# Optimization experiments

Hardware: AMD Instinct MI355X
Metric: run time of the kernel (lower is better)

## Reference

```python
import jax, jax.numpy as jnp
import numpy as np

PATCH, WIN = 3, 7


def _unfold(x, k):
    # torch F.unfold(x, k, padding=k//2), stride 1 -> [b, c, k*k, h, w]
    # channel-major ordering (c slowest, then kernel row, then kernel col)
    pad = k // 2
    b, c, h, w = x.shape
    xp = jnp.pad(x, ((0, 0), (0, 0), (pad, pad), (pad, pad)))
    return jnp.stack([xp[:, :, i:i + h, j:j + w]
                      for i in range(k) for j in range(k)], axis=2)


def _conv3(x, w, b=None):
    y = jax.lax.conv_general_dilated(x, w, (1, 1), [(1, 1), (1, 1)],
                                     dimension_numbers=('NCHW', 'OIHW', 'NCHW'))
    if b is not None:
        y = y + b[None, :, None, None]
    return y


def _head(u_feat, pan_feat, w_phi, w_theta, w_g, p, ws):
    # SelfAttention: windowed/patch neighborhood attention
    b, c, h, w = pan_feat.shape
    phi = jnp.einsum('oi,bihw->bohw', w_phi, pan_feat)
    theta = jnp.einsum('oi,bihw->bohw', w_theta, pan_feat)
    thp = _unfold(theta, p).reshape(b, c * p * p, h, w)        # [b,D,h,w]
    php = _unfold(phi, p).reshape(b, c * p * p, h, w)          # [b,D,h,w]
    phw = _unfold(php, ws)                                     # [b,D,K,h,w], K=ws*ws
    att = jax.nn.softmax(jnp.einsum('bdhw,bdkhw->bhwk', thp, phw), axis=-1)
    g = jnp.einsum('oi,bihw->bohw', w_g, u_feat)
    gw = _unfold(g, ws)                                        # [b,cu,K,h,w]
    return jnp.einsum('bhwk,bckhw->bchw', att, gw)


def _forward(u, pan, w_nlu, w_nlpan, g_phi, g_theta, g_g, s_phi, s_theta, s_g,
             m_phi, m_theta, m_g, mlp_w, mlp_b, w_resu, w_respan,
             rb0_w1, rb0_b1, rb0_w2, rb0_b2, rb1_w1, rb1_b1, rb1_w2, rb1_b2,
             rb2_w1, rb2_b1, rb2_w2, rb2_b2, w_recon):
    uf = _conv3(u, w_nlu)      # [b,5,h,w]
    pf = _conv3(pan, w_nlpan)  # [b,3,h,w]
    h1 = _head(uf, pf, g_phi, g_theta, g_g, PATCH, WIN)
    h2 = _head(uf, uf, s_phi, s_theta, s_g, 1, WIN)
    h3 = _head(uf, jnp.concatenate([uf, pf], axis=1), m_phi, m_theta, m_g, PATCH, WIN)
    # mlp: Linear(3,1) over stacked heads (last dim of size 3)
    att = h1 * mlp_w[0, 0] + h2 * mlp_w[0, 1] + h3 * mlp_w[0, 2] + mlp_b[0]
    ru = _conv3(u, w_resu)
    rp = _conv3(pan, w_respan)
    x = jnp.concatenate([att, ru, rp], axis=1)  # [b, fc+10, h, w]
    rbs = [(rb0_w1, rb0_b1, rb0_w2, rb0_b2),
           (rb1_w1, rb1_b1, rb1_w2, rb1_b2),
           (rb2_w1, rb2_b1, rb2_w2, rb2_b2)]
    for w1, b1, w2, b2 in rbs:
        f = jax.nn.relu(_conv3(x, w1, b1))
        f = _conv3(f, w2, b2)
        x = jax.nn.relu(f + x)
    return _conv3(x, w_recon)


def setup_inputs() -> dict:
    key = jax.random.key(0)
    ks = jax.random.split(key, 32)
    def n(i, shape, s=0.1):
        return jax.random.normal(ks[i], shape, dtype=jnp.float32) * s
    B, H, W = 1, 128, 128
    FC = 32
    C = FC + 10
    inp = {
        'u': jax.random.normal(ks[0], (B, 8, H, W), dtype=jnp.float32),
        'pan': jax.random.normal(ks[1], (B, 1, H, W), dtype=jnp.float32),
        'w_nlu': n(2, (5, 8, 3, 3)),
        'w_nlpan': n(3, (3, 1, 3, 3)),
        'g_phi': n(4, (3, 3)), 'g_theta': n(5, (3, 3)), 'g_g': n(6, (5, 5)),
        's_phi': n(7, (5, 5)), 's_theta': n(8, (5, 5)), 's_g': n(9, (5, 5)),
        'm_phi': n(10, (8, 8)), 'm_theta': n(11, (8, 8)), 'm_g': n(12, (5, 5)),
        'mlp_w': n(13, (1, 3), 0.5), 'mlp_b': n(14, (1,), 0.1),
        'w_resu': n(15, (FC, 8, 3, 3)), 'w_respan': n(16, (5, 1, 3, 3)),
        'w_recon': n(17, (8, C, 3, 3)),
    }
    k = 18
    for i in range(3):
        inp[f'rb{i}_w1'] = n(k, (C, C, 3, 3))
        inp[f'rb{i}_b1'] = n(k + 1, (C,), 0.01)
        inp[f'rb{i}_w2'] = n(k + 2, (C, C, 3, 3))
        inp[f'rb{i}_b2'] = n(k + 3, (C,), 0.01)
        k += 4
    return inp


def reference(u, pan, w_nlu, w_nlpan, g_phi, g_theta, g_g, s_phi, s_theta, s_g,
              m_phi, m_theta, m_g, mlp_w, mlp_b, w_resu, w_respan,
              rb0_w1, rb0_b1, rb0_w2, rb0_b2, rb1_w1, rb1_b1, rb1_w2, rb1_b2,
              rb2_w1, rb2_b1, rb2_w2, rb2_b2, w_recon):
    return _forward(u, pan, w_nlu, w_nlpan, g_phi, g_theta, g_g, s_phi, s_theta,
                    s_g, m_phi, m_theta, m_g, mlp_w, mlp_b, w_resu, w_respan,
                    rb0_w1, rb0_b1, rb0_w2, rb0_b2, rb1_w1, rb1_b1, rb1_w2,
                    rb1_b2, rb2_w1, rb2_b1, rb2_w2, rb2_b2, w_recon)
```

## Files before the change

kernel.cpp:

```cpp
#include <hip/hip_runtime.h>


#define DEV __device__ __forceinline__
typedef float f32x4 __attribute__((ext_vector_type(4)));
typedef __bf16 bf16x8 __attribute__((ext_vector_type(8)));
typedef unsigned short u16;
typedef unsigned int u32;

constexpr int N = 128 * 128;

constexpr int OFF_PHI1 =   0 * N;
constexpr int OFF_TH1  =   3 * N;
constexpr int OFF_PHI2 =   6 * N;
constexpr int OFF_TH2  =  11 * N;
constexpr int OFF_PHI3 =  16 * N;
constexpr int OFF_TH3  =  24 * N;
constexpr int OFF_G1   =  32 * N;
constexpr int OFF_G2   =  37 * N;
constexpr int OFF_G3   =  42 * N;
constexpr int OFF_X    =  47 * N;
constexpr int OFF_OH1  =  89 * N;
constexpr int OFF_OH2  =  94 * N;
constexpr int OFF_OH3  =  99 * N;
constexpr int XPLANE   = 130 * 136;
constexpr int OFF_XPAD = 110 * N;
constexpr int OFF_FPAD = 133 * N;
constexpr int OFF_SLAB = 156 * N;
constexpr int OFF_BTAB = 160 * N;
constexpr int SLAB_RB  = 18432;
constexpr int SLAB_RC  = 110592;
constexpr int SLAB_TOT = 116736;
constexpr int ZPB      = 528;
constexpr int ZTOT     = 2 * 42 * ZPB;
constexpr int WPREP_TOT = 384 + SLAB_TOT + ZTOT;
constexpr int WPREP_BLK = (WPREP_TOT + 255) / 256;

DEV bool inb(int y, int x) { return (unsigned)y < 128u && (unsigned)x < 128u; }
DEV u16 f2bf(float f) {
    unsigned u = __float_as_uint(f);
    return (u16)((u + 0x7fffu + ((u >> 16) & 1u)) >> 16);
}

struct PrepArgs {
    const float* u;    const float* pan;  const float* wnlu; const float* wnlpan;
    const float* gphi; const float* gth;  const float* gg;   const float* sphi;
    const float* sth;  const float* sg;   const float* mphi; const float* mth;
    const float* mg;
    const float* w[7];
};

__global__ __launch_bounds__(256) void prep_k(PrepArgs pa, float* __restrict__ ws,
                                              u16* __restrict__ slab,
                                              u16* __restrict__ btab,
                                              u16* __restrict__ xpad,
                                              u16* __restrict__ fpad) {
    const int bid = blockIdx.x, t = threadIdx.x;
    if (bid < 128) {
        const int p = (bid & 63) * 256 + t;
        const int y = p >> 7, x = p & 127;

        float uv[8][9];
#pragma unroll
        for (int ic = 0; ic < 8; ++ic)
#pragma unroll
            for (int i = 0; i < 3; ++i)
#pragma unroll
                for (int j = 0; j < 3; ++j) {
                    int yy = y + i - 1, xx = x + j - 1;
                    uv[ic][i * 3 + j] =
                        inb(yy, xx) ? pa.u[ic * N + yy * 128 + xx] : 0.f;
                }
        float uf[5] = {0, 0, 0, 0, 0};
#pragma unroll
        for (int ic = 0; ic < 8; ++ic)
#pragma unroll
            for (int k = 0; k < 9; ++k)
#pragma unroll
                for (int o = 0; o < 5; ++o)
                    uf[o] = fmaf(uv[ic][k], pa.wnlu[(o * 8 + ic) * 9 + k], uf[o]);

        if (bid < 64) {
#pragma unroll
            for (int o = 0; o < 5; ++o) {
                float a = 0, b = 0, c1 = 0, c2 = 0, c3 = 0;
#pragma unroll
                for (int i = 0; i < 5; ++i) {
                    a  = fmaf(pa.sphi[o * 5 + i], uf[i], a);
                    b  = fmaf(pa.sth [o * 5 + i], uf[i], b);
                    c1 = fmaf(pa.gg  [o * 5 + i], uf[i], c1);
                    c2 = fmaf(pa.sg  [o * 5 + i], uf[i], c2);
                    c3 = fmaf(pa.mg  [o * 5 + i], uf[i], c3);
                }
                ws[OFF_PHI2 + o * N + p] = a;
                ws[OFF_TH2  + o * N + p] = b;
                ws[OFF_G1   + o * N + p] = c1;
                ws[OFF_G2   + o * N + p] = c2;
                ws[OFF_G3   + o * N + p] = c3;
            }
        } else {
            float pv[9];
#pragma unroll
            for (int i = 0; i < 3; ++i)
#pragma unroll
                for (int j = 0; j < 3; ++j) {
                    int yy = y + i - 1, xx = x + j - 1;
                    pv[i * 3 + j] = inb(yy, xx) ? pa.pan[yy * 128 + xx] : 0.f;
                }
            float pf[3] = {0, 0, 0};
#pragma unroll
            for (int k = 0; k < 9; ++k)
#pragma unroll
                for (int o = 0; o < 3; ++o)
                    pf[o] = fmaf(pv[k], pa.wnlpan[o * 9 + k], pf[o]);
            float cat[8] = {uf[0], uf[1], uf[2], uf[3], uf[4],
                            pf[0], pf[1], pf[2]};
#pragma unroll
            for (int o = 0; o < 3; ++o) {
                float a = 0, b = 0;
#pragma unroll
                for (int i = 0; i < 3; ++i) {
                    a = fmaf(pa.gphi[o * 3 + i], pf[i], a);
                    b = fmaf(pa.gth [o * 3 + i], pf[i], b);
                }
                ws[OFF_PHI1 + o * N + p] = a;
                ws[OFF_TH1  + o * N + p] = b;
            }
#pragma unroll
            for (int o = 0; o < 8; ++o) {
                float a = 0, b = 0;
#pragma unroll
                for (int i = 0; i < 8; ++i) {
                    a = fmaf(pa.mphi[o * 8 + i], cat[i], a);
                    b = fmaf(pa.mth [o * 8 + i], cat[i], b);
                }
                ws[OFF_PHI3 + o * N + p] = a;
                ws[OFF_TH3  + o * N + p] = b;
            }
        }
        return;
    }

    int idx = (bid - 128) * 256 + t;
    if (idx >= WPREP_TOT) return;
    if (idx < 384) {
        u16 v = 0;
        if (idx < 378) {
            int ic = idx / 9, tau = idx - ic * 9;
            v = (u16)(ic * 120 + (tau / 3) * 40 + (tau % 3));
        }
        btab[idx] = v;
        return;
    }
    idx -= 384;
    if (idx < SLAB_TOT) {
        const float* W;
        int mt, ks, lane, j, ocv;
        if (idx < SLAB_RC) {
            int cv = idx / SLAB_RB, r = idx - cv * SLAB_RB;
            mt = r / 6144; r -= mt * 6144;
            ks = r / 512;  r -= ks * 512;
            lane = r / 8;  j = r - lane * 8;
            W = pa.w[cv]; ocv = 42;
        } else {
            int r = idx - SLAB_RC;
            mt = 0;
            ks = r / 512;  r -= ks * 512;
            lane = r / 8;  j = r - lane * 8;
            W = pa.w[6]; ocv = 8;
        }
        int k  = ks * 32 + (lane >> 4) * 8 + j;
        int oc = mt * 16 + (lane & 15);
        u16 v = 0;
        if (k < 378 && oc < ocv) {
            int ic = k / 9, tau = k - ic * 9;
            v = f2bf(W[(oc * 42 + ic) * 9 + tau]);
        }
        slab[idx] = v;
        return;
    }
    idx -= SLAB_TOT;
    u16* buf = (idx < 42 * ZPB) ? xpad : fpad;
    int e = (idx < 42 * ZPB) ? idx : idx - 42 * ZPB;
    int plane = e / ZPB, rem = e - plane * ZPB;
    int row, col;
    if (rem < 136)      { row = 0;             col = rem; }
    else if (rem < 272) { row = 129;           col = rem - 136; }
    else if (rem < 400) { row = 1 + rem - 272; col = 0; }
    else                { row = 1 + rem - 400; col = 129; }
    buf[plane * XPLANE + row * 136 + col] = 0;
}

template <int C, int P>
DEV void head_tile(const float* __restrict__ phi, const float* __restrict__ theta,
                   const float* __restrict__ g, float* __restrict__ oh,
                   float* __restrict__ smem, int ty0, int tx0, int t) {
    constexpr int PR  = P / 2;
    constexpr int H3  = 3 + PR;
    constexpr int W   = 6 + P;
    constexpr int TTH = 8 + 2 * PR, TTW = 8 + 2 * PR;
    constexpr int PTH = 8 + 2 * H3, PTW = 8 + 2 * H3;
    constexpr int GTH = 14, GTW = 14;

    float* sT = smem;
    float* sP = sT + C * TTH * TTW;
    float* sG = sP + C * PTH * PTW;

#pragma unroll
    for (int c = 0; c < C; ++c)
#pragma unroll
        for (int base = 0; base < TTH * TTW; base += 128) {
            int i = base + t;
            if (i < TTH * TTW) {
                int r = i / TTW, cc = i - r * TTW;
                int gy = ty0 - PR + r, gx = tx0 - PR + cc;
                sT[c * TTH * TTW + i] =
                    inb(gy, gx) ? theta[c * N + gy * 128 + gx] : 0.f;
            }
        }
#pragma unroll
    for (int c = 0; c < C; ++c)
#pragma unroll
        for (int base = 0; base < PTH * PTW; base += 128) {
            int i = base + t;
            if (i < PTH * PTW) {
                int r = i / PTW, cc = i - r * PTW;
                int gy = ty0 - H3 + r, gx = tx0 - H3 + cc;
                sP[c * PTH * PTW + i] =
                    inb(gy, gx) ? phi[c * N + gy * 128 + gx] : 0.f;
            }
        }
#pragma unroll
    for (int c = 0; c < 5; ++c)
#pragma unroll
        for (int base = 0; base < GTH * GTW; base += 128) {
            int i = base + t;
            if (i < GTH * GTW) {
                int r = i / GTW, cc = i - r * GTW;
                int gy = ty0 - 3 + r, gx = tx0 - 3 + cc;
                sG[c * GTH * GTW + i] =
                    inb(gy, gx) ? g[c * N + gy * 128 + gx] : 0.f;
            }
        }
    __syncthreads();

    const int wave = t >> 6, lane = t & 63, m = lane >> 5;
    const int pidx = (lane & 31) | (wave << 5);
    const int py = pidx >> 3, px = pidx & 7;
    const int gy = ty0 + py, gx = tx0 + px;
    const int dbase = m * 3;

    float s[28];
#pragma unroll
    for (int k = 0; k < 28; ++k) s[k] = 0.f;

    for (int c = 0; c < C; ++c) {
        const float* tc = sT + c * TTH * TTW;
        const float* pc = sP + c * PTH * PTW;
        float T[P][P];
#pragma unroll
        for (int i = 0; i < P; ++i)
#pragma unroll
            for (int j = 0; j < P; ++j)
                T[i][j] = tc[(py + i) * TTW + px + j];
        float R[P][W];
#pragma unroll
        for (int r = 0; r < P; ++r)
#pragma unroll
            for (int w = 0; w < W; ++w)
                R[r][w] = pc[(py + dbase + r) * PTW + px + w];
#pragma unroll
        for (int dd = 0; dd < 4; ++dd) {
#pragma unroll
            for (int dx = 0; dx < 7; ++dx) {
                float a = 0.f;
#pragma unroll
                for (int i = 0; i < P; ++i)
#pragma unroll
                    for (int j = 0; j < P; ++j)
                        a = fmaf(T[i][j], R[i][dx + j], a);
                s[dd * 7 + dx] += a;
            }
            if (dd < 3) {
#pragma unroll
                for (int r = 0; r < P - 1; ++r)
#pragma unroll
                    for (int w = 0; w < W; ++w) R[r][w] = R[r + 1][w];
                int row = py + dbase + dd + P;
#pragma unroll
                for (int w = 0; w < W; ++w)
                    R[P - 1][w] = pc[row * PTW + px + w];
            }
        }
    }
#pragma unroll
    for (int k = 0; k < 28; ++k) {
        int d = dbase + k / 7, dx = k % 7;
        if (!inb(gy + d - 3, gx + dx - 3)) s[k] = 0.f;
    }
    const bool half0 = (m == 0);
    float mx = -3.0e38f;
#pragma unroll
    for (int k = 0; k < 28; ++k) {
        bool own = half0 || (k >= 7);
        mx = own ? fmaxf(mx, s[k]) : mx;
    }
    mx = fmaxf(mx, __shfl_xor(mx, 32));
    float sum = 0.f;
#pragma unroll
    for (int k = 0; k < 28; ++k) {
        bool own = half0 || (k >= 7);
        float e = own ? __expf(s[k] - mx) : 0.f;
        s[k] = e;
        sum += e;
    }
    sum += __shfl_xor(sum, 32);

    float o[5] = {0, 0, 0, 0, 0};
#pragma unroll
    for (int k = 0; k < 28; ++k) {
        int d = dbase + k / 7, dx = k % 7;
        int gr = (py + d) * GTW + px + dx;
#pragma unroll
        for (int c5 = 0; c5 < 5; ++c5)
            o[c5] = fmaf(s[k], sG[c5 * GTH * GTW + gr], o[c5]);
    }
#pragma unroll
    for (int c5 = 0; c5 < 5; ++c5) o[c5] += __shfl_xor(o[c5], 32);

    if (half0) {
        float inv = 1.f / sum;
        int p = gy * 128 + gx;
#pragma unroll
        for (int c5 = 0; c5 < 5; ++c5) oh[c5 * N + p] = o[c5] * inv;
    }
}

__global__ __launch_bounds__(128) void heads_k(float* __restrict__ ws) {
    __shared__ float smem[3828];
    const int t = threadIdx.x;
    const int ty0 = (blockIdx.x >> 4) * 8, tx0 = (blockIdx.x & 15) * 8;
    if (blockIdx.y == 0)
        head_tile<3, 3>(ws + OFF_PHI1, ws + OFF_TH1, ws + OFF_G1, ws + OFF_OH1,
                        smem, ty0, tx0, t);
    else if (blockIdx.y == 1)
        head_tile<5, 1>(ws + OFF_PHI2, ws + OFF_TH2, ws + OFF_G2, ws + OFF_OH2,
                        smem, ty0, tx0, t);
    else
        head_tile<8, 3>(ws + OFF_PHI3, ws + OFF_TH3, ws + OFF_G3, ws + OFF_OH3,
                        smem, ty0, tx0, t);
}

__global__ __launch_bounds__(256, 2) void assemble_k(
    const float* __restrict__ u, const float* __restrict__ pan,
    const float* __restrict__ wres, const float* __restrict__ wrp,
    const float* __restrict__ mlpw, const float* __restrict__ mlpb,
    float* __restrict__ ws, u16* __restrict__ xpad) {
    const int p = blockIdx.x * 256 + threadIdx.x;
    const int y = p >> 7, x = p & 127;
    const int padp = (y + 1) * 136 + (x + 1);
    float* xb = ws + OFF_X;

    if (blockIdx.y == 0) {
        const float w0 = mlpw[0], w1 = mlpw[1], w2 = mlpw[2];
        const float bb = mlpb[0];
#pragma unroll
        for (int c = 0; c < 5; ++c) {
            float a = ws[OFF_OH1 + c * N + p] * w0 +
                      ws[OFF_OH2 + c * N + p] * w1 +
                      ws[OFF_OH3 + c * N + p] * w2 + bb;
            xb[c * N + p] = a;
            xpad[c * XPLANE + padp] = f2bf(a);
        }
        float pv[9];
#pragma unroll
        for (int i = 0; i < 3; ++i)
#pragma unroll
            for (int j = 0; j < 3; ++j) {
                int yy = y + i - 1, xx = x + j - 1;
                pv[i * 3 + j] = inb(yy, xx) ? pan[yy * 128 + xx] : 0.f;
            }
        float a5[5] = {0, 0, 0, 0, 0};
#pragma unroll
        for (int k = 0; k < 9; ++k)
#pragma unroll
            for (int o = 0; o < 5; ++o)
                a5[o] = fmaf(pv[k], wrp[o * 9 + k], a5[o]);
#pragma unroll
        for (int o = 0; o < 5; ++o) {
            xb[(37 + o) * N + p] = a5[o];
            xpad[(37 + o) * XPLANE + padp] = f2bf(a5[o]);
        }
    } else {
        const int ob = (blockIdx.y - 1) * 8;
        float uv[8][9];
#pragma unroll
        for (int ic = 0; ic < 8; ++ic)
#pragma unroll
            for (int i = 0; i < 3; ++i)
#pragma unroll
                for (int j = 0; j < 3; ++j) {
                    int yy = y + i - 1, xx = x + j - 1;
                    uv[ic][i * 3 + j] =
                        inb(yy, xx) ? u[ic * N + yy * 128 + xx] : 0.f;
                }
        float acc[8] = {0, 0, 0, 0, 0, 0, 0, 0};
#pragma unroll
        for (int ic = 0; ic < 8; ++ic)
#pragma unroll
            for (int k = 0; k < 9; ++k)
#pragma unroll
                for (int o = 0; o < 8; ++o)
                    acc[o] = fmaf(uv[ic][k], wres[((ob + o) * 8 + ic) * 9 + k],
                                  acc[o]);
#pragma unroll
        for (int o = 0; o < 8; ++o) {
            xb[(5 + ob + o) * N + p] = acc[o];
            xpad[(5 + ob + o) * XPLANE + padp] = f2bf(acc[o]);
        }
    }
}

template <int MT, int OCV, bool BIAS, bool RELU, bool SKIP, bool WF32, bool WPAD>
__global__ __launch_bounds__(128, 1) void convm_k(
    const u16* __restrict__ xin, const u16* __restrict__ slab,
    const u16* __restrict__ btab, const float* __restrict__ bs,
    const float* __restrict__ skip, float* __restrict__ of32,
    u16* __restrict__ opad) {
    __shared__ __align__(16) u16 sX[5040];
    __shared__ __align__(16) u16 sBt[384];
    const int t = threadIdx.x;
    const int y = blockIdx.x >> 2, x0 = (blockIdx.x & 3) << 5;

    const u16* srcbase = xin + y * 136 + x0;
#pragma unroll
    for (int it = 0; it < 5; ++it) {
        int c = it * 128 + t;
        if (c < 630) {
            int row = c / 5, slot = c - row * 5;
            int ic = row / 3, r = row - ic * 3;
            uint4 v = *((const uint4*)(srcbase + ic * XPLANE + r * 136) + slot);
            *(uint4*)(sX + row * 40 + slot * 8) = v;
        }
    }
#pragma unroll
    for (int it = 0; it < 3; ++it) sBt[it * 128 + t] = btab[it * 128 + t];
    __syncthreads();

    const int lane = t & 63, wave = t >> 6;
    const int quad = lane >> 4, col = lane & 15;
    const int ncol = wave * 16 + col;

    union AB { uint4 u; bf16x8 b; };
    AB a[MT][12];
#pragma unroll
    for (int mt = 0; mt < MT; ++mt)
#pragma unroll
        for (int ks = 0; ks < 12; ++ks)
            a[mt][ks].u = ((const uint4*)slab)[(mt * 12 + ks) * 64 + lane];

    f32x4 acc[MT];
#pragma unroll
    for (int mt = 0; mt < MT; ++mt) acc[mt] = {0.f, 0.f, 0.f, 0.f};

#pragma unroll
    for (int ks = 0; ks < 12; ++ks) {
        union { uint4 u; u16 s[8]; } off;
        off.u = *(const uint4*)(sBt + ks * 32 + quad * 8);
        union { u16 s[8]; bf16x8 b; } bv;
#pragma unroll
        for (int j = 0; j < 8; ++j) bv.s[j] = sX[off.s[j] + ncol];
#pragma unroll
        for (int mt = 0; mt < MT; ++mt)
            acc[mt] = __builtin_amdgcn_mfma_f32_16x16x32_bf16(
                a[mt][ks].b, bv.b, acc[mt], 0, 0, 0);
    }

    const int xg = x0 + ncol;
    const int px = y * 128 + xg;
    const int padp = (y + 1) * 136 + (xg + 1);
#pragma unroll
    for (int mt = 0; mt < MT; ++mt)
#pragma unroll
        for (int reg = 0; reg < 4; ++reg) {
            int oc = mt * 16 + quad * 4 + reg;
            if (oc < OCV) {
                float v = acc[mt][reg];
                if (BIAS) v += bs[oc];
                if (SKIP) v += skip[oc * N + px];
                if (RELU) v = fmaxf(v, 0.f);
                if (WF32) of32[oc * N + px] = v;
                if (WPAD) opad[oc * XPLANE + padp] = f2bf(v);
            }
        }
}

extern "C" void kernel_launch(void* const* d_in, const int* in_sizes, int n_in,
                              void* d_out, int out_size, void* d_ws, size_t ws_size,
                              hipStream_t stream) {
    (void)in_sizes; (void)n_in; (void)out_size; (void)ws_size;
    float* ws = (float*)d_ws;
    float* out = (float*)d_out;

    PrepArgs pa;
    pa.u      = (const float*)d_in[0];
    pa.pan    = (const float*)d_in[1];
    pa.wnlu   = (const float*)d_in[2];
    pa.wnlpan = (const float*)d_in[3];
    pa.gphi   = (const float*)d_in[4];
    pa.gth    = (const float*)d_in[5];
    pa.gg     = (const float*)d_in[6];
    pa.sphi   = (const float*)d_in[7];
    pa.sth    = (const float*)d_in[8];
    pa.sg     = (const float*)d_in[9];
    pa.mphi   = (const float*)d_in[10];
    pa.mth    = (const float*)d_in[11];
    pa.mg     = (const float*)d_in[12];
    pa.w[0]   = (const float*)d_in[18];
    pa.w[1]   = (const float*)d_in[20];
    pa.w[2]   = (const float*)d_in[22];
    pa.w[3]   = (const float*)d_in[24];
    pa.w[4]   = (const float*)d_in[26];
    pa.w[5]   = (const float*)d_in[28];
    pa.w[6]   = (const float*)d_in[17];

    const float* mlpw = (const float*)d_in[13];
    const float* mlpb = (const float*)d_in[14];
    const float* wres = (const float*)d_in[15];
    const float* wrp  = (const float*)d_in[16];

    u16* xpad = (u16*)(ws + OFF_XPAD);
    u16* fpad = (u16*)(ws + OFF_FPAD);
    u16* slab = (u16*)(ws + OFF_SLAB);
    u16* btab = (u16*)(ws + OFF_BTAB);

    prep_k<<<128 + WPREP_BLK, 256, 0, stream>>>(pa, ws, slab, btab, xpad, fpad);
    heads_k<<<dim3(256, 3), 128, 0, stream>>>(ws);
    assemble_k<<<dim3(64, 5), 256, 0, stream>>>(pa.u, pa.pan, wres, wrp, mlpw,
                                                mlpb, ws, xpad);

    for (int r = 0; r < 3; ++r) {
        const float* b1 = (const float*)d_in[19 + 4 * r];
        const float* b2 = (const float*)d_in[21 + 4 * r];
        convm_k<3, 42, true, true, false, false, true>
            <<<512, 128, 0, stream>>>(xpad, slab + (2 * r) * SLAB_RB, btab, b1,
                                      nullptr, nullptr, fpad);
        convm_k<3, 42, true, true, true, true, true>
            <<<512, 128, 0, stream>>>(fpad, slab + (2 * r + 1) * SLAB_RB, btab,
                                      b2, ws + OFF_X, ws + OFF_X, xpad);
    }
    convm_k<1, 8, false, false, false, true, false>
        <<<512, 128, 0, stream>>>(xpad, slab + SLAB_RC, btab, nullptr, nullptr,
                                  out, nullptr);
}
```

Baseline: 210.9 us.

## Fuse residual-block conv pairs and merge heads with assemble kernel

```diff
diff --git a/kernel.cpp b/kernel.cpp
--- a/kernel.cpp
+++ b/kernel.cpp
@@ -19,20 +19,17 @@
 constexpr int OFF_G2   =  37 * N;
 constexpr int OFF_G3   =  42 * N;
 constexpr int OFF_X    =  47 * N;
-constexpr int OFF_OH1  =  89 * N;
-constexpr int OFF_OH2  =  94 * N;
-constexpr int OFF_OH3  =  99 * N;
-constexpr int XPLANE   = 130 * 136;
-constexpr int OFF_XPAD = 110 * N;
-constexpr int OFF_FPAD = 133 * N;
-constexpr int OFF_SLAB = 156 * N;
-constexpr int OFF_BTAB = 160 * N;
+constexpr int XPLANE   = 132 * 144;
+constexpr int OFF_XPA  = 110 * N;
+constexpr int OFF_XPB  = 135 * N;
+constexpr int OFF_SLAB = 160 * N;
+constexpr int OFF_BTAB = 164 * N;
 constexpr int SLAB_RB  = 18432;
 constexpr int SLAB_RC  = 110592;
 constexpr int SLAB_TOT = 116736;
-constexpr int ZPB      = 528;
+constexpr int ZPB      = 2624;
 constexpr int ZTOT     = 2 * 42 * ZPB;
-constexpr int WPREP_TOT = 384 + SLAB_TOT + ZTOT;
+constexpr int WPREP_TOT = 1152 + SLAB_TOT + ZTOT;
 constexpr int WPREP_BLK = (WPREP_TOT + 255) / 256;
 
 DEV bool inb(int y, int x) { return (unsigned)y < 128u && (unsigned)x < 128u; }
@@ -52,8 +49,8 @@
 __global__ __launch_bounds__(256) void prep_k(PrepArgs pa, float* __restrict__ ws,
                                               u16* __restrict__ slab,
                                               u16* __restrict__ btab,
-                                              u16* __restrict__ xpad,
-                                              u16* __restrict__ fpad) {
+                                              u16* __restrict__ xpa,
+                                              u16* __restrict__ xpb) {
     const int bid = blockIdx.x, t = threadIdx.x;
     if (bid < 128) {
         const int p = (bid & 63) * 256 + t;
@@ -142,16 +139,19 @@
 
     int idx = (bid - 128) * 256 + t;
     if (idx >= WPREP_TOT) return;
-    if (idx < 384) {
+    if (idx < 1152) {
+        int which = idx / 384, k = idx - which * 384;
         u16 v = 0;
-        if (idx < 378) {
-            int ic = idx / 9, tau = idx - ic * 9;
-            v = (u16)(ic * 120 + (tau / 3) * 40 + (tau % 3));
+        if (k < 378) {
+            int ic = k / 9, tau = k - ic * 9, i = tau / 3, j = tau - i * 3;
+            if (which == 0)      v = (u16)(ic * 360 + i * 72 + j);
+            else if (which == 1) v = (u16)(ic * 216 + i * 72 + j);
+            else                 v = (u16)(ic * 120 + i * 40 + j + 1);
         }
         btab[idx] = v;
         return;
     }
-    idx -= 384;
+    idx -= 1152;
     if (idx < SLAB_TOT) {
         const float* W;
         int mt, ks, lane, j, ocv;
@@ -179,21 +179,27 @@
         return;
     }
     idx -= SLAB_TOT;
-    u16* buf = (idx < 42 * ZPB) ? xpad : fpad;
+    u16* buf = (idx < 42 * ZPB) ? xpa : xpb;
     int e = (idx < 42 * ZPB) ? idx : idx - 42 * ZPB;
     int plane = e / ZPB, rem = e - plane * ZPB;
     int row, col;
-    if (rem < 136)      { row = 0;             col = rem; }
-    else if (rem < 272) { row = 129;           col = rem - 136; }
-    else if (rem < 400) { row = 1 + rem - 272; col = 0; }
-    else                { row = 1 + rem - 400; col = 129; }
-    buf[plane * XPLANE + row * 136 + col] = 0;
+    if (rem < 576) {
+        int rr = rem / 144;
+        row = (rr < 2) ? rr : rr + 128;
+        col = rem - rr * 144;
+    } else {
+        int r2 = rem - 576;
+        row = 2 + r2 / 16;
+        int ci = r2 & 15;
+        col = (ci < 2) ? ci : 128 + ci;
+    }
+    buf[plane * XPLANE + row * 144 + col] = 0;
 }
 
 template <int C, int P>
 DEV void head_tile(const float* __restrict__ phi, const float* __restrict__ theta,
-                   const float* __restrict__ g, float* __restrict__ oh,
-                   float* __restrict__ smem, int ty0, int tx0, int t) {
+                   const float* __restrict__ g, float* __restrict__ smem,
+                   int ty0, int tx0, int t, float ohv[5]) {
     constexpr int PR  = P / 2;
     constexpr int H3  = 3 + PR;
     constexpr int W   = 6 + P;
@@ -205,6 +211,7 @@
     float* sP = sT + C * TTH * TTW;
     float* sG = sP + C * PTH * PTW;
 
+    __syncthreads();
 #pragma unroll
     for (int c = 0; c < C; ++c)
 #pragma unroll
@@ -327,56 +334,81 @@
 #pragma unroll
     for (int c5 = 0; c5 < 5; ++c5) o[c5] += __shfl_xor(o[c5], 32);
 
-    if (half0) {
-        float inv = 1.f / sum;
-        int p = gy * 128 + gx;
-#pragma unroll
-        for (int c5 = 0; c5 < 5; ++c5) oh[c5 * N + p] = o[c5] * inv;
-    }
+    float inv = 1.f / sum;
+#pragma unroll
+    for (int c5 = 0; c5 < 5; ++c5) ohv[c5] = o[c5] * inv;
 }
 
-__global__ __launch_bounds__(128) void heads_k(float* __restrict__ ws) {
-    __shared__ float smem[3828];
-    const int t = threadIdx.x;
-    const int ty0 = (blockIdx.x >> 4) * 8, tx0 = (blockIdx.x & 15) * 8;
-    if (blockIdx.y == 0)
-        head_tile<3, 3>(ws + OFF_PHI1, ws + OFF_TH1, ws + OFF_G1, ws + OFF_OH1,
-                        smem, ty0, tx0, t);
-    else if (blockIdx.y == 1)
-        head_tile<5, 1>(ws + OFF_PHI2, ws + OFF_TH2, ws + OFF_G2, ws + OFF_OH2,
-                        smem, ty0, tx0, t);
-    else
-        head_tile<8, 3>(ws + OFF_PHI3, ws + OFF_TH3, ws + OFF_G3, ws + OFF_OH3,
-                        smem, ty0, tx0, t);
-}
-
-__global__ __launch_bounds__(256, 2) void assemble_k(
+__global__ __launch_bounds__(128) void headsasm_k(
     const float* __restrict__ u, const float* __restrict__ pan,
     const float* __restrict__ wres, const float* __restrict__ wrp,
     const float* __restrict__ mlpw, const float* __restrict__ mlpb,
     float* __restrict__ ws, u16* __restrict__ xpad) {
-    const int p = blockIdx.x * 256 + threadIdx.x;
-    const int y = p >> 7, x = p & 127;
-    const int padp = (y + 1) * 136 + (x + 1);
+    __shared__ float smem[3828];
+    const int t = threadIdx.x;
+    const int ty0 = (blockIdx.x >> 4) * 8, tx0 = (blockIdx.x & 15) * 8;
+
+    float h1[5], h2[5], h3[5];
+    head_tile<3, 3>(ws + OFF_PHI1, ws + OFF_TH1, ws + OFF_G1, smem, ty0, tx0,
+                    t, h1);
+    head_tile<5, 1>(ws + OFF_PHI2, ws + OFF_TH2, ws + OFF_G2, smem, ty0, tx0,
+                    t, h2);
+    head_tile<8, 3>(ws + OFF_PHI3, ws + OFF_TH3, ws + OFF_G3, smem, ty0, tx0,
+                    t, h3);
+
+    const int wave = t >> 6, lane = t & 63, m = lane >> 5;
+    const int pidx = (lane & 31) | (wave << 5);
+    const int py = pidx >> 3, px8 = pidx & 7;
+    const int gy = ty0 + py, gx = tx0 + px8;
+    const int p = gy * 128 + gx;
+    const int padp = (gy + 2) * 144 + (gx + 2);
     float* xb = ws + OFF_X;
 
-    if (blockIdx.y == 0) {
+    if (m == 0) {
         const float w0 = mlpw[0], w1 = mlpw[1], w2 = mlpw[2];
         const float bb = mlpb[0];
 #pragma unroll
         for (int c = 0; c < 5; ++c) {
-            float a = ws[OFF_OH1 + c * N + p] * w0 +
-                      ws[OFF_OH2 + c * N + p] * w1 +
-                      ws[OFF_OH3 + c * N + p] * w2 + bb;
+            float a = h1[c] * w0 + h2[c] * w1 + h3[c] * w2 + bb;
             xb[c * N + p] = a;
             xpad[c * XPLANE + padp] = f2bf(a);
         }
+    }
+    float uv[8][9];
+#pragma unroll
+    for (int ic = 0; ic < 8; ++ic)
+#pragma unroll
+        for (int i = 0; i < 3; ++i)
+#pragma unroll
+            for (int j = 0; j < 3; ++j) {
+                int yy = gy + i - 1, xx = gx + j - 1;
+                uv[ic][i * 3 + j] = inb(yy, xx) ? u[ic * N + yy * 128 + xx] : 0.f;
+            }
+    const int ob = m * 16;
+    float acc[16];
+#pragma unroll
+    for (int o = 0; o < 16; ++o) acc[o] = 0.f;
+#pragma unroll
+    for (int ic = 0; ic < 8; ++ic)
+#pragma unroll
+        for (int k = 0; k < 9; ++k)
+#pragma unroll
+            for (int o = 0; o < 16; ++o)
+                acc[o] = fmaf(uv[ic][k], wres[((ob + o) * 8 + ic) * 9 + k],
+                              acc[o]);
+#pragma unroll
+    for (int o = 0; o < 16; ++o) {
+        int ch = 5 + ob + o;
+        xb[ch * N + p] = acc[o];
+        xpad[ch * XPLANE + padp] = f2bf(acc[o]);
+    }
+    if (m == 1) {
         float pv[9];
 #pragma unroll
         for (int i = 0; i < 3; ++i)
 #pragma unroll
             for (int j = 0; j < 3; ++j) {
-                int yy = y + i - 1, xx = x + j - 1;
+                int yy = gy + i - 1, xx = gx + j - 1;
                 pv[i * 3 + j] = inb(yy, xx) ? pan[yy * 128 + xx] : 0.f;
             }
         float a5[5] = {0, 0, 0, 0, 0};
@@ -387,63 +419,152 @@
                 a5[o] = fmaf(pv[k], wrp[o * 9 + k], a5[o]);
 #pragma unroll
         for (int o = 0; o < 5; ++o) {
-            xb[(37 + o) * N + p] = a5[o];
-            xpad[(37 + o) * XPLANE + padp] = f2bf(a5[o]);
-        }
-    } else {
-        const int ob = (blockIdx.y - 1) * 8;
-        float uv[8][9];
-#pragma unroll
-        for (int ic = 0; ic < 8; ++ic)
-#pragma unroll
-            for (int i = 0; i < 3; ++i)
-#pragma unroll
-                for (int j = 0; j < 3; ++j) {
-                    int yy = y + i - 1, xx = x + j - 1;
-                    uv[ic][i * 3 + j] =
-                        inb(yy, xx) ? u[ic * N + yy * 128 + xx] : 0.f;
+            int ch = 37 + o;
+            xb[ch * N + p] = a5[o];
+            xpad[ch * XPLANE + padp] = f2bf(a5[o]);
+        }
+    }
+}
+
+__global__ __launch_bounds__(128, 1) void rbfused_k(
+    const u16* __restrict__ xin, u16* __restrict__ xout,
+    const u16* __restrict__ slab1, const u16* __restrict__ slab2,
+    const u16* __restrict__ btab, const float* __restrict__ b1,
+    const float* __restrict__ b2, float* __restrict__ xskip) {
+    __shared__ __align__(16) u16 xT[15120];
+    __shared__ __align__(16) u16 fT[9072];
+    __shared__ __align__(16) u16 sBtA[384], sBtB[384];
+    __shared__ float sB1[42], sB2[42];
+    const int t = threadIdx.x;
+    const int y = blockIdx.x >> 1, x0 = (blockIdx.x & 1) << 6;
+
+#pragma unroll
+    for (int it = 0; it < 15; ++it) {
+        int c = it * 128 + t;
+        if (c < 1890) {
+            int row = c / 9, slot = c - row * 9;
+            int ic = row / 5, r5 = row - ic * 5;
+            uint4 v = *((const uint4*)(xin + ic * XPLANE + (y + r5) * 144 + x0)
+                        + slot);
+            *(uint4*)(xT + ic * 360 + r5 * 72 + slot * 8) = v;
+        }
+    }
+#pragma unroll
+    for (int it = 0; it < 3; ++it) sBtA[it * 128 + t] = btab[it * 128 + t];
+#pragma unroll
+    for (int it = 0; it < 3; ++it) sBtB[it * 128 + t] = btab[384 + it * 128 + t];
+    if (t < 42) { sB1[t] = b1[t]; sB2[t] = b2[t]; }
+    __syncthreads();
+
+    const int lane = t & 63, wave = t >> 6;
+    const int quad = lane >> 4, col = lane & 15;
+
+    union AB { uint4 u; bf16x8 b; };
+    AB a[3][12];
+#pragma unroll
+    for (int mt = 0; mt < 3; ++mt)
+#pragma unroll
+        for (int ks = 0; ks < 12; ++ks)
+            a[mt][ks].u = ((const uint4*)slab1)[(mt * 12 + ks) * 64 + lane];
+
+    for (int tl = wave; tl < 13; tl += 2) {
+        int n = tl * 16 + col;
+        bool valid = n < 198;
+        int r = n / 66, cc = n - r * 66;
+        int base = valid ? r * 72 + cc : 0;
+        f32x4 acc[3];
+#pragma unroll
+        for (int mt = 0; mt < 3; ++mt) acc[mt] = {0.f, 0.f, 0.f, 0.f};
+#pragma unroll
+        for (int ks = 0; ks < 12; ++ks) {
+            union { uint4 u; u16 s[8]; } off;
+            off.u = *(const uint4*)(sBtA + ks * 32 + quad * 8);
+            union { u16 s[8]; bf16x8 b; } bv;
+#pragma unroll
+            for (int j = 0; j < 8; ++j) bv.s[j] = xT[off.s[j] + base];
+#pragma unroll
+            for (int mt = 0; mt < 3; ++mt)
+                acc[mt] = __builtin_amdgcn_mfma_f32_16x16x32_bf16(
+                    a[mt][ks].b, bv.b, acc[mt], 0, 0, 0);
+        }
+        int gy = y - 1 + r, gx = x0 - 1 + cc;
+        bool img = inb(gy, gx);
+#pragma unroll
+        for (int mt = 0; mt < 3; ++mt)
+#pragma unroll
+            for (int reg = 0; reg < 4; ++reg) {
+                int oc = mt * 16 + quad * 4 + reg;
+                if (oc < 42 && valid) {
+                    float v = fmaxf(acc[mt][reg] + sB1[oc], 0.f);
+                    fT[oc * 216 + r * 72 + cc] = img ? f2bf(v) : (u16)0;
                 }
-        float acc[8] = {0, 0, 0, 0, 0, 0, 0, 0};
-#pragma unroll
-        for (int ic = 0; ic < 8; ++ic)
-#pragma unroll
-            for (int k = 0; k < 9; ++k)
-#pragma unroll
-                for (int o = 0; o < 8; ++o)
-                    acc[o] = fmaf(uv[ic][k], wres[((ob + o) * 8 + ic) * 9 + k],
-                                  acc[o]);
-#pragma unroll
-        for (int o = 0; o < 8; ++o) {
-            xb[(5 + ob + o) * N + p] = acc[o];
-            xpad[(5 + ob + o) * XPLANE + padp] = f2bf(acc[o]);
-        }
+            }
+    }
+    __syncthreads();
+
+#pragma unroll
+    for (int mt = 0; mt < 3; ++mt)
+#pragma unroll
+        for (int ks = 0; ks < 12; ++ks)
+            a[mt][ks].u = ((const uint4*)slab2)[(mt * 12 + ks) * 64 + lane];
+
+#pragma unroll
+    for (int ti = 0; ti < 2; ++ti) {
+        int ncol2 = (wave + 2 * ti) * 16 + col;
+        f32x4 acc[3];
+#pragma unroll
+        for (int mt = 0; mt < 3; ++mt) acc[mt] = {0.f, 0.f, 0.f, 0.f};
+#pragma unroll
+        for (int ks = 0; ks < 12; ++ks) {
+            union { uint4 u; u16 s[8]; } off;
+            off.u = *(const uint4*)(sBtB + ks * 32 + quad * 8);
+            union { u16 s[8]; bf16x8 b; } bv;
+#pragma unroll
+            for (int j = 0; j < 8; ++j) bv.s[j] = fT[off.s[j] + ncol2];
+#pragma unroll
+            for (int mt = 0; mt < 3; ++mt)
+                acc[mt] = __builtin_amdgcn_mfma_f32_16x16x32_bf16(
+                    a[mt][ks].b, bv.b, acc[mt], 0, 0, 0);
+        }
+        int xg = x0 + ncol2;
+        int px = y * 128 + xg;
+        int padp = (y + 2) * 144 + (xg + 2);
+#pragma unroll
+        for (int mt = 0; mt < 3; ++mt)
+#pragma unroll
+            for (int reg = 0; reg < 4; ++reg) {
+                int oc = mt * 16 + quad * 4 + reg;
+                if (oc < 42) {
+                    float v = acc[mt][reg] + sB2[oc] + xskip[oc * N + px];
+                    v = fmaxf(v, 0.f);
+                    xskip[oc * N + px] = v;
+                    xout[oc * XPLANE + padp] = f2bf(v);
+                }
+            }
     }
 }
 
-template <int MT, int OCV, bool BIAS, bool RELU, bool SKIP, bool WF32, bool WPAD>
-__global__ __launch_bounds__(128, 1) void convm_k(
+__global__ __launch_bounds__(128, 1) void convr_k(
     const u16* __restrict__ xin, const u16* __restrict__ slab,
-    const u16* __restrict__ btab, const float* __restrict__ bs,
-    const float* __restrict__ skip, float* __restrict__ of32,
-    u16* __restrict__ opad) {
+    const u16* __restrict__ btab, float* __restrict__ out) {
     __shared__ __align__(16) u16 sX[5040];
     __shared__ __align__(16) u16 sBt[384];
     const int t = threadIdx.x;
     const int y = blockIdx.x >> 2, x0 = (blockIdx.x & 3) << 5;
 
-    const u16* srcbase = xin + y * 136 + x0;
 #pragma unroll
     for (int it = 0; it < 5; ++it) {
         int c = it * 128 + t;
         if (c < 630) {
             int row = c / 5, slot = c - row * 5;
-            int ic = row / 3, r = row - ic * 3;
-            uint4 v = *((const uint4*)(srcbase + ic * XPLANE + r * 136) + slot);
+            int ic = row / 3, r3 = row - ic * 3;
+            uint4 v = *((const uint4*)(xin + ic * XPLANE + (y + 1 + r3) * 144
+                                       + x0) + slot);
             *(uint4*)(sX + row * 40 + slot * 8) = v;
         }
     }
 #pragma unroll
-    for (int it = 0; it < 3; ++it) sBt[it * 128 + t] = btab[it * 128 + t];
+    for (int it = 0; it < 3; ++it) sBt[it * 128 + t] = btab[768 + it * 128 + t];
     __syncthreads();
 
     const int lane = t & 63, wave = t >> 6;
@@ -451,17 +572,12 @@
     const int ncol = wave * 16 + col;
 
     union AB { uint4 u; bf16x8 b; };
-    AB a[MT][12];
-#pragma unroll
-    for (int mt = 0; mt < MT; ++mt)
-#pragma unroll
-        for (int ks = 0; ks < 12; ++ks)
-            a[mt][ks].u = ((const uint4*)slab)[(mt * 12 + ks) * 64 + lane];
-
-    f32x4 acc[MT];
-#pragma unroll
-    for (int mt = 0; mt < MT; ++mt) acc[mt] = {0.f, 0.f, 0.f, 0.f};
-
+    AB a[12];
+#pragma unroll
+    for (int ks = 0; ks < 12; ++ks)
+        a[ks].u = ((const uint4*)slab)[ks * 64 + lane];
+
+    f32x4 acc = {0.f, 0.f, 0.f, 0.f};
 #pragma unroll
     for (int ks = 0; ks < 12; ++ks) {
         union { uint4 u; u16 s[8]; } off;
@@ -469,29 +585,15 @@
         union { u16 s[8]; bf16x8 b; } bv;
 #pragma unroll
         for (int j = 0; j < 8; ++j) bv.s[j] = sX[off.s[j] + ncol];
-#pragma unroll
-        for (int mt = 0; mt < MT; ++mt)
-            acc[mt] = __builtin_amdgcn_mfma_f32_16x16x32_bf16(
-                a[mt][ks].b, bv.b, acc[mt], 0, 0, 0);
-    }
-
-    const int xg = x0 + ncol;
-    const int px = y * 128 + xg;
-    const int padp = (y + 1) * 136 + (xg + 1);
-#pragma unroll
-    for (int mt = 0; mt < MT; ++mt)
-#pragma unroll
-        for (int reg = 0; reg < 4; ++reg) {
-            int oc = mt * 16 + quad * 4 + reg;
-            if (oc < OCV) {
-                float v = acc[mt][reg];
-                if (BIAS) v += bs[oc];
-                if (SKIP) v += skip[oc * N + px];
-                if (RELU) v = fmaxf(v, 0.f);
-                if (WF32) of32[oc * N + px] = v;
-                if (WPAD) opad[oc * XPLANE + padp] = f2bf(v);
-            }
-        }
+        acc = __builtin_amdgcn_mfma_f32_16x16x32_bf16(a[ks].b, bv.b, acc,
+                                                      0, 0, 0);
+    }
+    const int px = y * 128 + x0 + ncol;
+#pragma unroll
+    for (int reg = 0; reg < 4; ++reg) {
+        int oc = quad * 4 + reg;
+        if (oc < 8) out[oc * N + px] = acc[reg];
+    }
 }
 
 extern "C" void kernel_launch(void* const* d_in, const int* in_sizes, int n_in,
@@ -528,27 +630,25 @@
     const float* wres = (const float*)d_in[15];
     const float* wrp  = (const float*)d_in[16];
 
-    u16* xpad = (u16*)(ws + OFF_XPAD);
-    u16* fpad = (u16*)(ws + OFF_FPAD);
+    u16* xpa  = (u16*)(ws + OFF_XPA);
+    u16* xpb  = (u16*)(ws + OFF_XPB);
     u16* slab = (u16*)(ws + OFF_SLAB);
     u16* btab = (u16*)(ws + OFF_BTAB);
 
-    prep_k<<<128 + WPREP_BLK, 256, 0, stream>>>(pa, ws, slab, btab, xpad, fpad);
-    heads_k<<<dim3(256, 3), 128, 0, stream>>>(ws);
-    assemble_k<<<dim3(64, 5), 256, 0, stream>>>(pa.u, pa.pan, wres, wrp, mlpw,
-                                                mlpb, ws, xpad);
-
-    for (int r = 0; r < 3; ++r) {
-        const float* b1 = (const float*)d_in[19 + 4 * r];
-        const float* b2 = (const float*)d_in[21 + 4 * r];
-        convm_k<3, 42, true, true, false, false, true>
-            <<<512, 128, 0, stream>>>(xpad, slab + (2 * r) * SLAB_RB, btab, b1,
-                                      nullptr, nullptr, fpad);
-        convm_k<3, 42, true, true, true, true, true>
-            <<<512, 128, 0, stream>>>(fpad, slab + (2 * r + 1) * SLAB_RB, btab,
-                                      b2, ws + OFF_X, ws + OFF_X, xpad);
-    }
-    convm_k<1, 8, false, false, false, true, false>
-        <<<512, 128, 0, stream>>>(xpad, slab + SLAB_RC, btab, nullptr, nullptr,
-                                  out, nullptr);
+    prep_k<<<128 + WPREP_BLK, 256, 0, stream>>>(pa, ws, slab, btab, xpa, xpb);
+    headsasm_k<<<256, 128, 0, stream>>>(pa.u, pa.pan, wres, wrp, mlpw, mlpb,
+                                        ws, xpa);
+    rbfused_k<<<256, 128, 0, stream>>>(xpa, xpb, slab + 0 * SLAB_RB,
+                                       slab + 1 * SLAB_RB, btab,
+                                       (const float*)d_in[19],
+                                       (const float*)d_in[21], ws + OFF_X);
+    rbfused_k<<<256, 128, 0, stream>>>(xpb, xpa, slab + 2 * SLAB_RB,
+                                       slab + 3 * SLAB_RB, btab,
+                                       (const float*)d_in[23],
+                                       (const float*)d_in[25], ws + OFF_X);
+    rbfused_k<<<256, 128, 0, stream>>>(xpa, xpb, slab + 4 * SLAB_RB,
+                                       slab + 5 * SLAB_RB, btab,
+                                       (const float*)d_in[27],
+                                       (const float*)d_in[29], ws + OFF_X);
+    convr_k<<<512, 128, 0, stream>>>(xpb, slab + SLAB_RC, btab, out);
 }
```

After: 297.6 us. 1.41x slower.

## Raise thread-level parallelism across prep, heads and residual conv kernels

Applied to the files above, without the earlier changes.

```diff
diff --git a/kernel.cpp b/kernel.cpp
--- a/kernel.cpp
+++ b/kernel.cpp
@@ -55,7 +55,8 @@
                                               u16* __restrict__ xpad,
                                               u16* __restrict__ fpad) {
     const int bid = blockIdx.x, t = threadIdx.x;
-    if (bid < 128) {
+    if (bid < 256) {
+        const int g = bid >> 6;
         const int p = (bid & 63) * 256 + t;
         const int y = p >> 7, x = p & 127;
 
@@ -79,23 +80,31 @@
                 for (int o = 0; o < 5; ++o)
                     uf[o] = fmaf(uv[ic][k], pa.wnlu[(o * 8 + ic) * 9 + k], uf[o]);
 
-        if (bid < 64) {
+        if (g == 0) {
 #pragma unroll
             for (int o = 0; o < 5; ++o) {
-                float a = 0, b = 0, c1 = 0, c2 = 0, c3 = 0;
+                float a = 0, b = 0, c1 = 0;
 #pragma unroll
                 for (int i = 0; i < 5; ++i) {
                     a  = fmaf(pa.sphi[o * 5 + i], uf[i], a);
                     b  = fmaf(pa.sth [o * 5 + i], uf[i], b);
                     c1 = fmaf(pa.gg  [o * 5 + i], uf[i], c1);
-                    c2 = fmaf(pa.sg  [o * 5 + i], uf[i], c2);
-                    c3 = fmaf(pa.mg  [o * 5 + i], uf[i], c3);
                 }
                 ws[OFF_PHI2 + o * N + p] = a;
                 ws[OFF_TH2  + o * N + p] = b;
                 ws[OFF_G1   + o * N + p] = c1;
-                ws[OFF_G2   + o * N + p] = c2;
-                ws[OFF_G3   + o * N + p] = c3;
+            }
+        } else if (g == 1) {
+#pragma unroll
+            for (int o = 0; o < 5; ++o) {
+                float c2 = 0, c3 = 0;
+#pragma unroll
+                for (int i = 0; i < 5; ++i) {
+                    c2 = fmaf(pa.sg[o * 5 + i], uf[i], c2);
+                    c3 = fmaf(pa.mg[o * 5 + i], uf[i], c3);
+                }
+                ws[OFF_G2 + o * N + p] = c2;
+                ws[OFF_G3 + o * N + p] = c3;
             }
         } else {
             float pv[9];
@@ -114,33 +123,41 @@
                     pf[o] = fmaf(pv[k], pa.wnlpan[o * 9 + k], pf[o]);
             float cat[8] = {uf[0], uf[1], uf[2], uf[3], uf[4],
                             pf[0], pf[1], pf[2]};
-#pragma unroll
-            for (int o = 0; o < 3; ++o) {
-                float a = 0, b = 0;
-#pragma unroll
-                for (int i = 0; i < 3; ++i) {
-                    a = fmaf(pa.gphi[o * 3 + i], pf[i], a);
-                    b = fmaf(pa.gth [o * 3 + i], pf[i], b);
-                }
-                ws[OFF_PHI1 + o * N + p] = a;
-                ws[OFF_TH1  + o * N + p] = b;
+            if (g == 2) {
+#pragma unroll
+                for (int o = 0; o < 3; ++o) {
+                    float a = 0, b = 0;
+#pragma unroll
+                    for (int i = 0; i < 3; ++i) {
+                        a = fmaf(pa.gphi[o * 3 + i], pf[i], a);
+                        b = fmaf(pa.gth [o * 3 + i], pf[i], b);
+                    }
+                    ws[OFF_PHI1 + o * N + p] = a;
+                    ws[OFF_TH1  + o * N + p] = b;
+                }
+#pragma unroll
+                for (int o = 0; o < 8; ++o) {
+                    float a = 0;
+#pragma unroll
+                    for (int i = 0; i < 8; ++i)
+                        a = fmaf(pa.mphi[o * 8 + i], cat[i], a);
+                    ws[OFF_PHI3 + o * N + p] = a;
+                }
+            } else {
+#pragma unroll
+                for (int o = 0; o < 8; ++o) {
+                    float b = 0;
+#pragma unroll
+                    for (int i = 0; i < 8; ++i)
+                        b = fmaf(pa.mth[o * 8 + i], cat[i], b);
+                    ws[OFF_TH3 + o * N + p] = b;
+                }
             }
-#pragma unroll
-            for (int o = 0; o < 8; ++o) {
-                float a = 0, b = 0;
-#pragma unroll
-                for (int i = 0; i < 8; ++i) {
-                    a = fmaf(pa.mphi[o * 8 + i], cat[i], a);
-                    b = fmaf(pa.mth [o * 8 + i], cat[i], b);
-                }
-                ws[OFF_PHI3 + o * N + p] = a;
-                ws[OFF_TH3  + o * N + p] = b;
-            }
         }
         return;
     }
 
-    int idx = (bid - 128) * 256 + t;
+    int idx = (bid - 256) * 256 + t;
     if (idx >= WPREP_TOT) return;
     if (idx < 384) {
         u16 v = 0;
@@ -200,68 +217,68 @@
     constexpr int TTH = 8 + 2 * PR, TTW = 8 + 2 * PR;
     constexpr int PTH = 8 + 2 * H3, PTW = 8 + 2 * H3;
     constexpr int GTH = 14, GTW = 14;
+    constexpr int CH0 = (C + 1) / 2;
 
     float* sT = smem;
     float* sP = sT + C * TTH * TTW;
     float* sG = sP + C * PTH * PTW;
 
 #pragma unroll
-    for (int c = 0; c < C; ++c)
-#pragma unroll
-        for (int base = 0; base < TTH * TTW; base += 128) {
-            int i = base + t;
-            if (i < TTH * TTW) {
-                int r = i / TTW, cc = i - r * TTW;
-                int gy = ty0 - PR + r, gx = tx0 - PR + cc;
-                sT[c * TTH * TTW + i] =
-                    inb(gy, gx) ? theta[c * N + gy * 128 + gx] : 0.f;
-            }
-        }
-#pragma unroll
-    for (int c = 0; c < C; ++c)
-#pragma unroll
-        for (int base = 0; base < PTH * PTW; base += 128) {
-            int i = base + t;
-            if (i < PTH * PTW) {
-                int r = i / PTW, cc = i - r * PTW;
-                int gy = ty0 - H3 + r, gx = tx0 - H3 + cc;
-                sP[c * PTH * PTW + i] =
-                    inb(gy, gx) ? phi[c * N + gy * 128 + gx] : 0.f;
-            }
-        }
-#pragma unroll
-    for (int c = 0; c < 5; ++c)
-#pragma unroll
-        for (int base = 0; base < GTH * GTW; base += 128) {
-            int i = base + t;
-            if (i < GTH * GTW) {
-                int r = i / GTW, cc = i - r * GTW;
-                int gy = ty0 - 3 + r, gx = tx0 - 3 + cc;
-                sG[c * GTH * GTW + i] =
-                    inb(gy, gx) ? g[c * N + gy * 128 + gx] : 0.f;
-            }
-        }
+    for (int c = 0; c < C; ++c) {
+        int i = t;
+        if (i < TTH * TTW) {
+            int r = i / TTW, cc = i - r * TTW;
+            int gy = ty0 - PR + r, gx = tx0 - PR + cc;
+            sT[c * TTH * TTW + i] =
+                inb(gy, gx) ? theta[c * N + gy * 128 + gx] : 0.f;
+        }
+    }
+#pragma unroll
+    for (int c = 0; c < C; ++c) {
+        int i = t;
+        if (i < PTH * PTW) {
+            int r = i / PTW, cc = i - r * PTW;
+            int gy = ty0 - H3 + r, gx = tx0 - H3 + cc;
+            sP[c * PTH * PTW + i] =
+                inb(gy, gx) ? phi[c * N + gy * 128 + gx] : 0.f;
+        }
+    }
+#pragma unroll
+    for (int c = 0; c < 5; ++c) {
+        int i = t;
+        if (i < GTH * GTW) {
+            int r = i / GTW, cc = i - r * GTW;
+            int gy = ty0 - 3 + r, gx = tx0 - 3 + cc;
+            sG[c * GTH * GTW + i] =
+                inb(gy, gx) ? g[c * N + gy * 128 + gx] : 0.f;
+        }
+    }
     __syncthreads();
 
-    const int wave = t >> 6, lane = t & 63, m = lane >> 5;
-    const int pidx = (lane & 31) | (wave << 5);
+    const int lane = t & 63, wave = t >> 6;
+    const int h = (lane >> 4) & 1, m = lane >> 5;
+    const int pidx = wave * 16 + (lane & 15);
     const int py = pidx >> 3, px = pidx & 7;
     const int gy = ty0 + py, gx = tx0 + px;
     const int dbase = m * 3;
+    const int cbeg = h ? CH0 : 0, cend = h ? C : CH0;
 
     float s[28];
 #pragma unroll
     for (int k = 0; k < 28; ++k) s[k] = 0.f;
 
-    for (int c = 0; c < C; ++c) {
-        const float* tc = sT + c * TTH * TTW;
-        const float* pc = sP + c * PTH * PTW;
+#pragma unroll
+    for (int ci = 0; ci < CH0; ++ci) {
+        int c = cbeg + ci;
+        bool cok = c < cend;
+        const float* tc = sT + (cok ? c : 0) * TTH * TTW;
+        const float* pc = sP + (cok ? c : 0) * PTH * PTW;
         float T[P][P];
 #pragma unroll
         for (int i = 0; i < P; ++i)
 #pragma unroll
             for (int j = 0; j < P; ++j)
-                T[i][j] = tc[(py + i) * TTW + px + j];
+                T[i][j] = cok ? tc[(py + i) * TTW + px + j] : 0.f;
         float R[P][W];
 #pragma unroll
         for (int r = 0; r < P; ++r)
@@ -293,6 +310,9 @@
         }
     }
 #pragma unroll
+    for (int k = 0; k < 28; ++k) s[k] += __shfl_xor(s[k], 16);
+
+#pragma unroll
     for (int k = 0; k < 28; ++k) {
         int d = dbase + k / 7, dx = k % 7;
         if (!inb(gy + d - 3, gx + dx - 3)) s[k] = 0.f;
@@ -315,27 +335,30 @@
     }
     sum += __shfl_xor(sum, 32);
 
-    float o[5] = {0, 0, 0, 0, 0};
+    const int gb = h ? 3 : 0, gn = h ? 2 : 3;
+    float o[3] = {0, 0, 0};
 #pragma unroll
     for (int k = 0; k < 28; ++k) {
         int d = dbase + k / 7, dx = k % 7;
         int gr = (py + d) * GTW + px + dx;
 #pragma unroll
-        for (int c5 = 0; c5 < 5; ++c5)
-            o[c5] = fmaf(s[k], sG[c5 * GTH * GTW + gr], o[c5]);
-    }
-#pragma unroll
-    for (int c5 = 0; c5 < 5; ++c5) o[c5] += __shfl_xor(o[c5], 32);
+        for (int c5 = 0; c5 < 3; ++c5)
+            if (c5 < gn)
+                o[c5] = fmaf(s[k], sG[(gb + c5) * GTH * GTW + gr], o[c5]);
+    }
+#pragma unroll
+    for (int c5 = 0; c5 < 3; ++c5) o[c5] += __shfl_xor(o[c5], 32);
 
     if (half0) {
         float inv = 1.f / sum;
         int p = gy * 128 + gx;
 #pragma unroll
-        for (int c5 = 0; c5 < 5; ++c5) oh[c5 * N + p] = o[c5] * inv;
-    }
-}
-
-__global__ __launch_bounds__(128) void heads_k(float* __restrict__ ws) {
+        for (int c5 = 0; c5 < 3; ++c5)
+            if (c5 < gn) oh[(gb + c5) * N + p] = o[c5] * inv;
+    }
+}
+
+__global__ __launch_bounds__(256) void heads_k(float* __restrict__ ws) {
     __shared__ float smem[3828];
     const int t = threadIdx.x;
     const int ty0 = (blockIdx.x >> 4) * 8, tx0 = (blockIdx.x & 15) * 8;
@@ -420,8 +443,8 @@
     }
 }
 
-template <int MT, int OCV, bool BIAS, bool RELU, bool SKIP, bool WF32, bool WPAD>
-__global__ __launch_bounds__(128, 1) void convm_k(
+template <bool SKIP, bool WF32, bool WPAD>
+__global__ __launch_bounds__(384, 3) void convm_k(
     const u16* __restrict__ xin, const u16* __restrict__ slab,
     const u16* __restrict__ btab, const float* __restrict__ bs,
     const float* __restrict__ skip, float* __restrict__ of32,
@@ -433,6 +456,67 @@
 
     const u16* srcbase = xin + y * 136 + x0;
 #pragma unroll
+    for (int it = 0; it < 2; ++it) {
+        int c = it * 384 + t;
+        if (c < 630) {
+            int row = c / 5, slot = c - row * 5;
+            int ic = row / 3, r = row - ic * 3;
+            uint4 v = *((const uint4*)(srcbase + ic * XPLANE + r * 136) + slot);
+            *(uint4*)(sX + row * 40 + slot * 8) = v;
+        }
+    }
+    sBt[t >= 384 ? 0 : t] = btab[t >= 384 ? 0 : t];
+    __syncthreads();
+
+    const int lane = t & 63, wave = t >> 6;
+    const int ph = wave / 3, mt = wave - ph * 3;
+    const int quad = lane >> 4, col = lane & 15;
+    const int ncol = ph * 16 + col;
+
+    union AB { uint4 u; bf16x8 b; };
+    AB a[12];
+#pragma unroll
+    for (int ks = 0; ks < 12; ++ks)
+        a[ks].u = ((const uint4*)slab)[(mt * 12 + ks) * 64 + lane];
+
+    f32x4 acc = {0.f, 0.f, 0.f, 0.f};
+#pragma unroll
+    for (int ks = 0; ks < 12; ++ks) {
+        union { uint4 u; u16 s[8]; } off;
+        off.u = *(const uint4*)(sBt + ks * 32 + quad * 8);
+        union { u16 s[8]; bf16x8 b; } bv;
+#pragma unroll
+        for (int j = 0; j < 8; ++j) bv.s[j] = sX[off.s[j] + ncol];
+        acc = __builtin_amdgcn_mfma_f32_16x16x32_bf16(a[ks].b, bv.b, acc,
+                                                      0, 0, 0);
+    }
+
+    const int xg = x0 + ncol;
+    const int px = y * 128 + xg;
+    const int padp = (y + 1) * 136 + (xg + 1);
+#pragma unroll
+    for (int reg = 0; reg < 4; ++reg) {
+        int oc = mt * 16 + quad * 4 + reg;
+        if (oc < 42) {
+            float v = acc[reg] + bs[oc];
+            if (SKIP) v += skip[oc * N + px];
+            v = fmaxf(v, 0.f);
+            if (WF32) of32[oc * N + px] = v;
+            if (WPAD) opad[oc * XPLANE + padp] = f2bf(v);
+        }
+    }
+}
+
+__global__ __launch_bounds__(128, 1) void convr_k(
+    const u16* __restrict__ xin, const u16* __restrict__ slab,
+    const u16* __restrict__ btab, float* __restrict__ out) {
+    __shared__ __align__(16) u16 sX[5040];
+    __shared__ __align__(16) u16 sBt[384];
+    const int t = threadIdx.x;
+    const int y = blockIdx.x >> 2, x0 = (blockIdx.x & 3) << 5;
+
+    const u16* srcbase = xin + y * 136 + x0;
+#pragma unroll
     for (int it = 0; it < 5; ++it) {
         int c = it * 128 + t;
         if (c < 630) {
@@ -451,17 +535,12 @@
     const int ncol = wave * 16 + col;
 
     union AB { uint4 u; bf16x8 b; };
-    AB a[MT][12];
-#pragma unroll
-    for (int mt = 0; mt < MT; ++mt)
-#pragma unroll
-        for (int ks = 0; ks < 12; ++ks)
-            a[mt][ks].u = ((const uint4*)slab)[(mt * 12 + ks) * 64 + lane];
-
-    f32x4 acc[MT];
-#pragma unroll
-    for (int mt = 0; mt < MT; ++mt) acc[mt] = {0.f, 0.f, 0.f, 0.f};
-
+    AB a[12];
+#pragma unroll
+    for (int ks = 0; ks < 12; ++ks)
+        a[ks].u = ((const uint4*)slab)[ks * 64 + lane];
+
+    f32x4 acc = {0.f, 0.f, 0.f, 0.f};
 #pragma unroll
     for (int ks = 0; ks < 12; ++ks) {
         union { uint4 u; u16 s[8]; } off;
@@ -469,29 +548,15 @@
         union { u16 s[8]; bf16x8 b; } bv;
 #pragma unroll
         for (int j = 0; j < 8; ++j) bv.s[j] = sX[off.s[j] + ncol];
-#pragma unroll
-        for (int mt = 0; mt < MT; ++mt)
-            acc[mt] = __builtin_amdgcn_mfma_f32_16x16x32_bf16(
-                a[mt][ks].b, bv.b, acc[mt], 0, 0, 0);
-    }
-
-    const int xg = x0 + ncol;
-    const int px = y * 128 + xg;
-    const int padp = (y + 1) * 136 + (xg + 1);
-#pragma unroll
-    for (int mt = 0; mt < MT; ++mt)
-#pragma unroll
-        for (int reg = 0; reg < 4; ++reg) {
-            int oc = mt * 16 + quad * 4 + reg;
-            if (oc < OCV) {
-                float v = acc[mt][reg];
-                if (BIAS) v += bs[oc];
-                if (SKIP) v += skip[oc * N + px];
-                if (RELU) v = fmaxf(v, 0.f);
-                if (WF32) of32[oc * N + px] = v;
-                if (WPAD) opad[oc * XPLANE + padp] = f2bf(v);
-            }
-        }
+        acc = __builtin_amdgcn_mfma_f32_16x16x32_bf16(a[ks].b, bv.b, acc,
+                                                      0, 0, 0);
+    }
+    const int px = y * 128 + x0 + ncol;
+#pragma unroll
+    for (int reg = 0; reg < 4; ++reg) {
+        int oc = quad * 4 + reg;
+        if (oc < 8) out[oc * N + px] = acc[reg];
+    }
 }
 
 extern "C" void kernel_launch(void* const* d_in, const int* in_sizes, int n_in,
@@ -533,22 +598,20 @@
     u16* slab = (u16*)(ws + OFF_SLAB);
     u16* btab = (u16*)(ws + OFF_BTAB);
 
-    prep_k<<<128 + WPREP_BLK, 256, 0, stream>>>(pa, ws, slab, btab, xpad, fpad);
-    heads_k<<<dim3(256, 3), 128, 0, stream>>>(ws);
+    prep_k<<<256 + WPREP_BLK, 256, 0, stream>>>(pa, ws, slab, btab, xpad, fpad);
+    heads_k<<<dim3(256, 3), 256, 0, stream>>>(ws);
     assemble_k<<<dim3(64, 5), 256, 0, stream>>>(pa.u, pa.pan, wres, wrp, mlpw,
                                                 mlpb, ws, xpad);
 
     for (int r = 0; r < 3; ++r) {
         const float* b1 = (const float*)d_in[19 + 4 * r];
         const float* b2 = (const float*)d_in[21 + 4 * r];
-        convm_k<3, 42, true, true, false, false, true>
-            <<<512, 128, 0, stream>>>(xpad, slab + (2 * r) * SLAB_RB, btab, b1,
+        convm_k<false, false, true>
+            <<<512, 384, 0, stream>>>(xpad, slab + (2 * r) * SLAB_RB, btab, b1,
                                       nullptr, nullptr, fpad);
-        convm_k<3, 42, true, true, true, true, true>
-            <<<512, 128, 0, stream>>>(fpad, slab + (2 * r + 1) * SLAB_RB, btab,
+        convm_k<true, true, true>
+            <<<512, 384, 0, stream>>>(fpad, slab + (2 * r + 1) * SLAB_RB, btab,
                                       b2, ws + OFF_X, ws + OFF_X, xpad);
     }
-    convm_k<1, 8, false, false, false, true, false>
-        <<<512, 128, 0, stream>>>(xpad, slab + SLAB_RC, btab, nullptr, nullptr,
-                                  out, nullptr);
-}
+    convr_k<<<512, 128, 0, stream>>>(xpad, slab + SLAB_RC, btab, out);
+}
```

Result: no change. 208.9 us (median of 2 runs) (-0.9%).
